# Optimization experiments

Measured on AMD Instinct MI355X. Metric: run time of the kernel, lower is better.

## Reference

```python
import jax, jax.numpy as jnp
import numpy as np

N = 50000      # nodes
E = 800000     # edges
D_IN = 128     # irreps_in dim
SH = 16        # irreps_sh dim (lmax=3)
EA = 16        # edge_attr_dim
H = 8          # num_heads
DQ = 64        # irreps_query dim (8 per head)
DK = 64        # irreps_key dim (8 per head)
DV = 128       # irreps_out dim (16 per head)
HID = 64       # radial MLP hidden


def setup_inputs() -> dict:
    key = jax.random.key(0)
    ks = jax.random.split(key, 20)
    g = lambda k, shape, fan: jax.random.normal(k, shape, jnp.float32) / np.sqrt(fan)
    return {
        "node_attr": jax.random.normal(ks[0], (N, D_IN), jnp.float32),
        "edge_attr": jax.random.normal(ks[1], (E, EA), jnp.float32),
        "edge_sh": jax.random.normal(ks[2], (E, SH), jnp.float32),
        # h_q linear
        "Wq": g(ks[3], (D_IN, DQ), D_IN),
        # h_k conv: depthwise SH mixing, channel-mixing linear, radial MLP gate
        "Wang_k": g(ks[4], (D_IN, SH), SH),
        "Wlin_k": g(ks[5], (D_IN, DK), D_IN),
        "W1k": g(ks[6], (EA, HID), EA),
        "b1k": jnp.zeros((HID,), jnp.float32),
        "W2k": g(ks[7], (HID, DK), HID),
        # h_v conv
        "Wang_v": g(ks[8], (D_IN, SH), SH),
        "Wlin_v": g(ks[9], (D_IN, DV), D_IN),
        "W1v": g(ks[10], (EA, HID), EA),
        "b1v": jnp.zeros((HID,), jnp.float32),
        "W2v": g(ks[11], (HID, DV), HID),
        # FullyConnectedTensorProduct(query_per_head, key_per_head, '0e') -> weighted bilinear dot
        "Wdot": g(ks[12], (DQ // H, DK // H), DQ // H),
        # lin_out
        "Wout": g(ks[13], (DV, DV), DV),
        "edge_index": jax.random.randint(ks[14], (2, E), 0, N, jnp.int64),
    }


def _conv_per_edge(x_src, edge_attr, edge_sh, Wang, Wlin, W1, b1, W2):
    # depthwise tensor product of node feats with edge SH, channel mix, radial gate
    rad = jax.nn.relu(edge_attr @ W1 + b1) @ W2          # [E, Dout]
    g = edge_sh @ Wang.T                                  # [E, D_IN]
    return ((x_src * g) @ Wlin) * rad                     # [E, Dout]


def reference(node_attr, edge_attr, edge_sh, Wq, Wang_k, Wlin_k, W1k, b1k, W2k,
              Wang_v, Wlin_v, W1v, b1v, W2v, Wdot, Wout, edge_index):
    src, dst = edge_index[0], edge_index[1]
    n = node_attr.shape[0]
    e = src.shape[0]

    q = (node_attr @ Wq).reshape(n, H, DQ // H)           # [N,H,dq]
    x_src = node_attr[src]                                # gather [E,D_IN]
    k = _conv_per_edge(x_src, edge_attr, edge_sh, Wang_k, Wlin_k, W1k, b1k, W2k).reshape(e, H, DK // H)
    v = _conv_per_edge(x_src, edge_attr, edge_sh, Wang_v, Wlin_v, W1v, b1v, W2v).reshape(e, H, DV // H)

    # TP 'dot' to scalars: weighted bilinear per head
    alpha = jnp.einsum('ehq,qk,ehk->eh', q[dst], Wdot, k)  # [E,H]

    # scatter_softmax over incoming edges of each dst node
    amax = jax.ops.segment_max(alpha, dst, num_segments=n)  # [N,H]
    ealpha = jnp.exp(alpha - amax[dst])
    denom = jax.ops.segment_sum(ealpha, dst, num_segments=n)
    attn = ealpha / denom[dst]                              # [E,H]

    # weighted scatter-sum of values
    out = jax.ops.segment_sum(attn[..., None] * v, dst, num_segments=n)  # [N,H,dv]
    return out.reshape(n, DV) @ Wout
```

## Files before the change

kernel.cpp:

```cpp
#include <hip/hip_runtime.h>
#include <stdint.h>

#define NN 50000
#define NE 800000
#define STRIP 49

typedef unsigned int u32;
typedef uint16_t u16;

__device__ __forceinline__ float b2f(u16 u){ return __builtin_bit_cast(float, (u32)((u32)u << 16)); }
__device__ __forceinline__ float b2f_lo(u32 p){ return __builtin_bit_cast(float, p << 16); }
__device__ __forceinline__ float b2f_hi(u32 p){ return __builtin_bit_cast(float, p & 0xffff0000u); }
__device__ __forceinline__ u32 f2b_bits(float f){ u32 u = __builtin_bit_cast(u32, f); return (u + 0x7fffu + ((u >> 16) & 1u)) >> 16; }
__device__ __forceinline__ u16 f2b(float f){ return (u16)f2b_bits(f); }
__device__ __forceinline__ u32 packb(float lo, float hi){
  u32 r;
  asm("v_cvt_pk_bf16_f32 %0, %1, %2" : "=v"(r) : "v"(lo), "v"(hi));
  return r;
}

typedef __bf16 bf16x2 __attribute__((ext_vector_type(2)));
#if defined(__has_builtin)
#if __has_builtin(__builtin_amdgcn_fdot2_f32_bf16)
#define HAVE_DOT2_BUILTIN 1
#endif
#endif

#ifdef HAVE_DOT2_BUILTIN
__device__ __forceinline__ float dot2b(u32 a, u32 b, float c){
  return __builtin_amdgcn_fdot2_f32_bf16(__builtin_bit_cast(bf16x2, a),
                                         __builtin_bit_cast(bf16x2, b), c, false);
}
#else
__device__ __forceinline__ float dot2b(u32 a, u32 b, float c){
  c = fmaf(b2f_lo(a), b2f_lo(b), c);
  return fmaf(b2f_hi(a), b2f_hi(b), c);
}
#endif

typedef __attribute__((ext_vector_type(8))) short short8;
typedef __attribute__((ext_vector_type(4))) float f32x4;
__device__ __forceinline__ f32x4 mf32(uint4 a, uint4 b, f32x4 c){
  return __builtin_amdgcn_mfma_f32_16x16x32_bf16(
      __builtin_bit_cast(short8, a), __builtin_bit_cast(short8, b), c, 0, 0, 0);
}

__device__ __forceinline__ int chperm(int n){
  return 32 * ((n & 63) >> 4) + 8 * ((n & 15) >> 2) + 4 * (n >> 6) + (n & 3);
}

#define OFF_WANG_V 0
#define OFF_W1_V   5120
#define OFF_WLIN_V 7680
#define OFF_W2_V   25088
#define OFF_WANG_K 34304
#define OFF_W1_K   39424
#define OFF_WLIN_K 41984
#define OFF_W2_K   50688
#define OFF_WOUT   55296
#define OFF_WQD    72704
#define WT_TOTAL   81408

__global__ __launch_bounds__(256) void zero_kernel(int* __restrict__ counts)
{
  int i = blockIdx.x * 256 + threadIdx.x;
  if (i < NN) counts[i] = 0;
}

__global__ __launch_bounds__(256) void prep_w_kernel(
    const float* __restrict__ Wang_v, const float* __restrict__ W1_v,
    const float* __restrict__ Wlin_v, const float* __restrict__ W2_v,
    const float* __restrict__ Wang_k, const float* __restrict__ W1_k,
    const float* __restrict__ Wlin_k, const float* __restrict__ W2_k,
    const float* __restrict__ Wout, const float* __restrict__ Wq,
    const float* __restrict__ Wdot,
    u16* __restrict__ wt)
{
  int idx = blockIdx.x * 256 + threadIdx.x;
  if (idx >= WT_TOTAL) return;
  float val = 0.f;
  if (idx < OFF_W1_V) {
    int l = idx - OFF_WANG_V, n = l / 40, k = l % 40;
    if (k >= 16 && k < 32) val = Wang_v[chperm(n) * 16 + (k - 16)];
  } else if (idx < OFF_WLIN_V) {
    int l = idx - OFF_W1_V, n = l / 40, k = l % 40;
    if (k < 16) val = W1_v[k * 64 + n];
  } else if (idx < OFF_W2_V) {
    int l = idx - OFF_WLIN_V, n = l / 136, k = l % 136;
    if (k < 128) val = Wlin_v[k * 128 + chperm(n)];
  } else if (idx < OFF_WANG_K) {
    int l = idx - OFF_W2_V, n = l / 72, k = l % 72;
    if (k < 64) val = W2_v[k * 128 + chperm(n)];
  } else if (idx < OFF_W1_K) {
    int l = idx - OFF_WANG_K, n = l / 40, k = l % 40;
    if (k >= 16 && k < 32) val = Wang_k[chperm(n) * 16 + (k - 16)];
  } else if (idx < OFF_WLIN_K) {
    int l = idx - OFF_W1_K, n = l / 40, k = l % 40;
    if (k < 16) val = W1_k[k * 64 + n];
  } else if (idx < OFF_W2_K) {
    int l = idx - OFF_WLIN_K, n = l / 136, k = l % 136;
    if (k < 128) val = Wlin_k[k * 64 + n];
  } else if (idx < OFF_WOUT) {
    int l = idx - OFF_W2_K, n = l / 72, k = l % 72;
    if (k < 64) val = W2_k[k * 64 + n];
  } else if (idx < OFF_WQD) {
    int l = idx - OFF_WOUT, n = l / 136, k = l % 136;
    if (k < 128) val = Wout[k * 128 + n];
  } else {
    int l = idx - OFF_WQD, n = l / 136, k = l % 136;
    if (k < 128) {
      int h = n >> 3, r = n & 7;
      float s = 0.f;
#pragma unroll
      for (int i = 0; i < 8; ++i) s += Wq[k * 64 + h * 8 + i] * Wdot[i * 8 + r];
      val = s;
    }
  }
  wt[idx] = f2b(val);
}

__global__ __launch_bounds__(256) void qw_kernel(const float* __restrict__ node_attr,
                                                 const u16* __restrict__ wt,
                                                 u16* __restrict__ qw)
{
  __shared__ __align__(16) u16 sX[64 * 136];
  uint4* sX4 = (uint4*)sX;
  u32* sX32 = (u32*)sX;
  const uint4* wt4 = (const uint4*)wt;
  const int tid = threadIdx.x, wv = tid >> 6, lane = tid & 63, lq = lane >> 4, ln = lane & 15;
  const int n0 = blockIdx.x * 64;
  uint4 rB[4];
#pragma unroll
  for (int ks = 0; ks < 4; ++ks) rB[ks] = wt4[9088 + (wv * 16 + ln) * 17 + ks * 4 + lq];
  {
    int row = tid >> 2, q4 = tid & 3;
    int n = n0 + row;
    bool valid = n < NN;
    const float4* xp = (const float4*)(node_attr + (size_t)(valid ? n : 0) * 128);
#pragma unroll
    for (int i = 0; i < 8; ++i) {
      float4 v = valid ? xp[q4 * 8 + i] : make_float4(0.f, 0.f, 0.f, 0.f);
      sX32[row * 68 + (q4 * 8 + i) * 2]     = packb(v.x, v.y);
      sX32[row * 68 + (q4 * 8 + i) * 2 + 1] = packb(v.z, v.w);
    }
  }
  __syncthreads();
  const f32x4 z4 = {0.f, 0.f, 0.f, 0.f};
  int col = wv * 16 + ln;
#pragma unroll
  for (int et = 0; et < 4; ++et) {
    f32x4 acc = z4;
#pragma unroll
    for (int ks = 0; ks < 4; ++ks) acc = mf32(sX4[(et * 16 + ln) * 17 + ks * 4 + lq], rB[ks], acc);
#pragma unroll
    for (int r = 0; r < 4; ++r) {
      int rr = n0 + et * 16 + lq * 4 + r;
      if (rr < NN) qw[(size_t)rr * 64 + col] = f2b(acc[r]);
    }
  }
}

__global__ __launch_bounds__(256) void count_kernel(const int* __restrict__ edge_index,
                                                    int* __restrict__ counts)
{
  int e = blockIdx.x * 256 + threadIdx.x;
  if (e < NE) { int d = edge_index[NE + e]; if ((u32)d >= NN) d = 0; atomicAdd(&counts[d], 1); }
}

__global__ __launch_bounds__(1024) void scan_kernel(const int* __restrict__ counts,
                                                    int* __restrict__ row_ptr,
                                                    int* __restrict__ cursor)
{
  __shared__ int s[1024];
  int tid = threadIdx.x;
  int base = tid * STRIP;
  int sum = 0;
  for (int i = 0; i < STRIP; ++i) { int idx = base + i; sum += (idx < NN) ? counts[idx] : 0; }
  s[tid] = sum;
  __syncthreads();
  for (int off = 1; off < 1024; off <<= 1) {
    int v = s[tid];
    int add = (tid >= off) ? s[tid - off] : 0;
    __syncthreads();
    s[tid] = v + add;
    __syncthreads();
  }
  int running = (tid == 0) ? 0 : s[tid - 1];
  for (int i = 0; i < STRIP; ++i) {
    int idx = base + i;
    if (idx < NN) { row_ptr[idx] = running; cursor[idx] = running; running += counts[idx]; }
  }
  if (tid == 1023) row_ptr[NN] = running;
}

__global__ __launch_bounds__(256) void fill_kernel(const int* __restrict__ edge_index,
                                                   int* __restrict__ cursor,
                                                   int* __restrict__ edge_pos)
{
  int e = blockIdx.x * 256 + threadIdx.x;
  if (e < NE) {
    int dst = edge_index[NE + e]; if ((u32)dst >= NN) dst = 0;
    int pos = atomicAdd(&cursor[dst], 1);
    edge_pos[e] = ((u32)pos < NE) ? pos : 0;
  }
}

__global__ __launch_bounds__(256, 2) void conv_fused_kernel(
    const float* __restrict__ node_attr, const float* __restrict__ edge_attr,
    const float* __restrict__ edge_sh, const int* __restrict__ edge_index,
    const float* __restrict__ b1v, const float* __restrict__ b1k,
    const u16* __restrict__ wt, const u16* __restrict__ qw,
    const int* __restrict__ edge_pos,
    u16* __restrict__ v_out, float* __restrict__ alpha)
{
  __shared__ __align__(16) u16 sC[64 * 40];
  __shared__ __align__(16) u16 sX[64 * 136];
  __shared__ __align__(16) u16 sTk[64 * 136];
  __shared__ __align__(16) u16 sHv[64 * 72];
  __shared__ __align__(16) u16 sHk[64 * 72];
  uint4* sC4 = (uint4*)sC; u32* sC32 = (u32*)sC;
  uint4* sX4 = (uint4*)sX;
  uint4* sTk4 = (uint4*)sTk;
  uint4* sHv4 = (uint4*)sHv;
  uint4* sHk4 = (uint4*)sHk;
  const uint4* wt4 = (const uint4*)wt;

  const int tid = threadIdx.x;
  const int wv = tid >> 6, lane = tid & 63, lq = lane >> 4, ln = lane & 15;
  const int e0 = blockIdx.x * 64;
  const int nA = wv * 16 + ln, nB = (wv + 4) * 16 + ln;
  const int cb  = wv * 16 + 4 * lq;
  const int cb8 = wv * 32 + 8 * lq;

  const int el = tid >> 2, p = tid & 3;
  int dq = edge_index[NE + e0 + el]; if ((u32)dq >= NN) dq = 0;
  const uint4* qptr = (const uint4*)(qw + (size_t)dq * 64 + p * 16);
  uint4 q0 = qptr[0], q1 = qptr[1];
  int pos_el = edge_pos[e0 + el]; if ((u32)pos_el >= NE) pos_el = 0;

  int srcs[4];
#pragma unroll
  for (int et = 0; et < 4; ++et) {
    int s = edge_index[e0 + et * 16 + ln];
    if ((u32)s >= NN) s = 0;
    srcs[et] = s;
  }

  uint4 rW1V    = wt4[640 + nA * 5 + lq];
  uint4 rW1K    = wt4[4928 + nA * 5 + lq];
  uint4 rWangV0 = wt4[nA * 5 + lq],        rWangV1 = wt4[nB * 5 + lq];
  uint4 rWangK0 = wt4[4288 + nA * 5 + lq], rWangK1 = wt4[4288 + nB * 5 + lq];
  float4 bV = *(const float4*)(b1v + cb);
  float4 bK = *(const float4*)(b1k + cb);

  {
    int r = tid >> 2, kq = tid & 3;
    float4 ea = ((const float4*)(edge_attr + (size_t)(e0 + r) * 16))[kq];
    *(uint2*)(sC32 + r * 20 + kq * 2) = make_uint2(packb(ea.x, ea.y), packb(ea.z, ea.w));
    float4 sh = ((const float4*)(edge_sh + (size_t)(e0 + r) * 16))[kq];
    *(uint2*)(sC32 + r * 20 + 8 + kq * 2) = make_uint2(packb(sh.x, sh.y), packb(sh.z, sh.w));
  }
  const float* xp0 = node_attr + (size_t)srcs[0] * 128 + cb8;
  float4 xa = *(const float4*)xp0;
  float4 xb = *(const float4*)(xp0 + 4);
  __syncthreads();

  const f32x4 z4 = {0.f, 0.f, 0.f, 0.f};
#pragma unroll
  for (int et = 0; et < 4; ++et) {
    float4 xa_n, xb_n;
    if (et < 3) {
      const float* xp = node_attr + (size_t)srcs[et + 1] * 128 + cb8;
      xa_n = *(const float4*)xp;
      xb_n = *(const float4*)(xp + 4);
    }
    uint4 aC = sC4[(et * 16 + ln) * 5 + lq];
    f32x4 hv  = mf32(rW1V, aC, z4);
    f32x4 hk  = mf32(rW1K, aC, z4);
    f32x4 t0v = mf32(rWangV0, aC, z4);
    f32x4 t1v = mf32(rWangV1, aC, z4);
    f32x4 t0k = mf32(rWangK0, aC, z4);
    f32x4 t1k = mf32(rWangK1, aC, z4);
    const int edge = et * 16 + ln;
    sX4[edge * 17 + 4 * wv + lq] = make_uint4(
        packb(t0v[0] * xa.x, t0v[1] * xa.y), packb(t0v[2] * xa.z, t0v[3] * xa.w),
        packb(t1v[0] * xb.x, t1v[1] * xb.y), packb(t1v[2] * xb.z, t1v[3] * xb.w));
    sTk4[edge * 17 + 4 * wv + lq] = make_uint4(
        packb(t0k[0] * xa.x, t0k[1] * xa.y), packb(t0k[2] * xa.z, t0k[3] * xa.w),
        packb(t1k[0] * xb.x, t1k[1] * xb.y), packb(t1k[2] * xb.z, t1k[3] * xb.w));
    *(uint2*)(sHv + edge * 72 + cb) = make_uint2(
        packb(fmaxf(hv[0] + bV.x, 0.f), fmaxf(hv[1] + bV.y, 0.f)),
        packb(fmaxf(hv[2] + bV.z, 0.f), fmaxf(hv[3] + bV.w, 0.f)));
    *(uint2*)(sHk + edge * 72 + cb) = make_uint2(
        packb(fmaxf(hk[0] + bK.x, 0.f), fmaxf(hk[1] + bK.y, 0.f)),
        packb(fmaxf(hk[2] + bK.z, 0.f), fmaxf(hk[3] + bK.w, 0.f)));
    xa = xa_n; xb = xb_n;
  }

  uint4 rWlinV[2][4], rWlinK[4], rW2V[2][2], rW2K[2];
#pragma unroll
  for (int ks = 0; ks < 4; ++ks) {
    rWlinV[0][ks] = wt4[960 + nA * 17 + ks * 4 + lq];
    rWlinV[1][ks] = wt4[960 + nB * 17 + ks * 4 + lq];
    rWlinK[ks]    = wt4[5248 + nA * 17 + ks * 4 + lq];
  }
#pragma unroll
  for (int ks = 0; ks < 2; ++ks) {
    rW2V[0][ks] = wt4[3136 + nA * 9 + ks * 4 + lq];
    rW2V[1][ks] = wt4[3136 + nB * 9 + ks * 4 + lq];
    rW2K[ks]    = wt4[6336 + nA * 9 + ks * 4 + lq];
  }
  __syncthreads();

  uint4 pv[4]; uint2 pk[4];
#pragma unroll
  for (int et = 0; et < 4; ++et) {
    const int er = et * 16 + ln;
    f32x4 acc0 = z4, acc1 = z4, acck = z4;
#pragma unroll
    for (int ks = 0; ks < 4; ++ks) {
      uint4 tb = sX4[er * 17 + ks * 4 + lq];
      acc0 = mf32(rWlinV[0][ks], tb, acc0);
      acc1 = mf32(rWlinV[1][ks], tb, acc1);
      acck = mf32(rWlinK[ks], sTk4[er * 17 + ks * 4 + lq], acck);
    }
    f32x4 b0 = z4, b1 = z4, bk = z4;
#pragma unroll
    for (int ks = 0; ks < 2; ++ks) {
      uint4 hb = sHv4[er * 9 + ks * 4 + lq];
      b0 = mf32(rW2V[0][ks], hb, b0);
      b1 = mf32(rW2V[1][ks], hb, b1);
      bk = mf32(rW2K[ks], sHk4[er * 9 + ks * 4 + lq], bk);
    }
    pv[et] = make_uint4(packb(acc0[0] * b0[0], acc0[1] * b0[1]),
                        packb(acc0[2] * b0[2], acc0[3] * b0[3]),
                        packb(acc1[0] * b1[0], acc1[1] * b1[1]),
                        packb(acc1[2] * b1[2], acc1[3] * b1[3]));
    pk[et] = make_uint2(packb(acck[0] * bk[0], acck[1] * bk[1]),
                        packb(acck[2] * bk[2], acck[3] * bk[3]));
  }
  __syncthreads();

#pragma unroll
  for (int et = 0; et < 4; ++et) {
    const int edge = et * 16 + ln;
    sX4[edge * 17 + 4 * wv + lq] = pv[et];
    *(uint2*)(sHk + edge * 72 + cb) = pk[et];
  }
  __syncthreads();

  {
    int row = tid >> 2, seg = tid & 3;
    uint4* gp = (uint4*)(v_out + (size_t)pos_el * 128);
#pragma unroll
    for (int i = 0; i < 4; ++i) gp[seg * 4 + i] = sX4[row * 17 + seg * 4 + i];
  }
  {
    uint4 k0 = sHk4[el * 9 + p * 2];
    uint4 k1 = sHk4[el * 9 + p * 2 + 1];
    float a0 = 0.f, a1 = 0.f;
    a0 = dot2b(q0.x, k0.x, a0); a0 = dot2b(q0.y, k0.y, a0);
    a0 = dot2b(q0.z, k0.z, a0); a0 = dot2b(q0.w, k0.w, a0);
    a1 = dot2b(q1.x, k1.x, a1); a1 = dot2b(q1.y, k1.y, a1);
    a1 = dot2b(q1.z, k1.z, a1); a1 = dot2b(q1.w, k1.w, a1);
    ((float2*)(alpha + (size_t)pos_el * 8))[p] = make_float2(a0, a1);
  }
}

#define OUPD(aa, ww)                                                   \
  { float mn = fmaxf(m, (aa));                                         \
    float sc = __expf(m - mn);                                         \
    float pw = __expf((aa) - mn);                                      \
    l = l * sc + pw;                                                   \
    accA = accA * sc + pw * b2f_lo(ww);                                \
    accB = accB * sc + pw * b2f_hi(ww);                                \
    m = mn; }

__global__ __launch_bounds__(256) void out_kernel(
    const int* __restrict__ row_ptr,
    const float* __restrict__ alpha, const u16* __restrict__ v_e,
    const u16* __restrict__ wt, float* __restrict__ out)
{
  __shared__ __align__(16) u16 sAgg[16 * 136];
  u32* sAgg32 = (u32*)sAgg;
  uint4* sAgg4 = (uint4*)sAgg;
  const uint4* wt4 = (const uint4*)wt;
  const u32* v32 = (const u32*)v_e;
  const int tid = threadIdx.x, wv = tid >> 6, lane = tid & 63, lq = lane >> 4, ln = lane & 15;
  const f32x4 z4 = {0.f, 0.f, 0.f, 0.f};
  uint4 rWT[2][4];
#pragma unroll
  for (int c = 0; c < 2; ++c) {
    int n = (wv * 2 + c) * 16 + ln;
#pragma unroll
    for (int ks = 0; ks < 4; ++ks) rWT[c][ks] = wt4[6912 + n * 17 + ks * 4 + lq];
  }
  const int hh = lane >> 3;
  const int grp = blockIdx.x;
#pragma unroll 1
  for (int i = 0; i < 4; ++i) {
    int n = grp * 16 + wv * 4 + i;
    int beg = row_ptr[n], end = row_ptr[n + 1];
    if (beg < 0) beg = 0; if (beg > NE) beg = NE;
    if (end < beg) end = beg; if (end > NE) end = NE;
    int deg = end - beg;
    float m = -3.0e38f, l = 0.f, accA = 0.f, accB = 0.f;
    int j = 0;
#pragma unroll 1
    for (; j + 4 <= deg; j += 4) {
      size_t b = (size_t)(beg + j);
      float a0 = alpha[(b)     * 8 + hh]; u32 w0 = v32[(b)     * 64 + lane];
      float a1 = alpha[(b + 1) * 8 + hh]; u32 w1 = v32[(b + 1) * 64 + lane];
      float a2 = alpha[(b + 2) * 8 + hh]; u32 w2 = v32[(b + 2) * 64 + lane];
      float a3 = alpha[(b + 3) * 8 + hh]; u32 w3 = v32[(b + 3) * 64 + lane];
      OUPD(a0, w0); OUPD(a1, w1); OUPD(a2, w2); OUPD(a3, w3);
    }
#pragma unroll 1
    for (; j < deg; ++j) {
      size_t b = (size_t)(beg + j);
      float a = alpha[b * 8 + hh]; u32 w = v32[b * 64 + lane];
      OUPD(a, w);
    }
    float inv = (l > 0.f) ? (1.f / l) : 0.f;
    accA *= inv; accB *= inv;
    sAgg32[(wv * 4 + i) * 68 + lane] = packb(accA, accB);
  }
  __syncthreads();
#pragma unroll
  for (int c = 0; c < 2; ++c) {
    f32x4 acc = z4;
#pragma unroll
    for (int ks = 0; ks < 4; ++ks) acc = mf32(sAgg4[ln * 17 + ks * 4 + lq], rWT[c][ks], acc);
    int col = (wv * 2 + c) * 16 + ln;
#pragma unroll
    for (int r = 0; r < 4; ++r)
      out[(size_t)(grp * 16 + lq * 4 + r) * 128 + col] = acc[r];
  }
}

extern "C" void kernel_launch(void* const* d_in, const int* in_sizes, int n_in,
                              void* d_out, int out_size, void* d_ws, size_t ws_size,
                              hipStream_t stream)
{
  const float* node_attr = (const float*)d_in[0];
  const float* edge_attr = (const float*)d_in[1];
  const float* edge_sh   = (const float*)d_in[2];
  const float* Wq        = (const float*)d_in[3];
  const float* Wang_k    = (const float*)d_in[4];
  const float* Wlin_k    = (const float*)d_in[5];
  const float* W1k       = (const float*)d_in[6];
  const float* b1k       = (const float*)d_in[7];
  const float* W2k       = (const float*)d_in[8];
  const float* Wang_v    = (const float*)d_in[9];
  const float* Wlin_v    = (const float*)d_in[10];
  const float* W1v       = (const float*)d_in[11];
  const float* b1v       = (const float*)d_in[12];
  const float* W2v       = (const float*)d_in[13];
  const float* Wdot      = (const float*)d_in[14];
  const float* Wout      = (const float*)d_in[15];
  const int* edge_index  = (const int*)d_in[16];
  float* out = (float*)d_out;

  char* ws = (char*)d_ws;
  u16*   v_e      = (u16*)(ws + 0);
  float* alpha    = (float*)(ws + 204800000);
  u16*   qw       = (u16*)(ws + 230400000);
  int*   counts   = (int*)(ws + 236800000);
  int*   row_ptr  = (int*)(ws + 237000064);
  int*   cursor   = (int*)(ws + 237200128);
  int*   edge_pos = (int*)(ws + 237400192);
  u16*   wt       = (u16*)(ws + 240600192);

  zero_kernel<<<dim3((NN + 255) / 256), dim3(256), 0, stream>>>(counts);
  prep_w_kernel<<<dim3((WT_TOTAL + 255) / 256), dim3(256), 0, stream>>>(
      Wang_v, W1v, Wlin_v, W2v, Wang_k, W1k, Wlin_k, W2k, Wout, Wq, Wdot, wt);
  qw_kernel<<<dim3((NN + 63) / 64), dim3(256), 0, stream>>>(node_attr, wt, qw);
  count_kernel<<<dim3((NE + 255) / 256), dim3(256), 0, stream>>>(edge_index, counts);
  scan_kernel<<<dim3(1), dim3(1024), 0, stream>>>(counts, row_ptr, cursor);
  fill_kernel<<<dim3((NE + 255) / 256), dim3(256), 0, stream>>>(edge_index, cursor, edge_pos);
  conv_fused_kernel<<<dim3(NE / 64), dim3(256), 0, stream>>>(
      node_attr, edge_attr, edge_sh, edge_index, b1v, b1k, wt, qw, edge_pos, v_e, alpha);
  out_kernel<<<dim3(3125), dim3(256), 0, stream>>>(row_ptr, alpha, v_e, wt, out);
}
```

Before: 642.6 us.

## Load edge attr/sh MFMA operands directly into registers, drop staging LDS buffer

Each lane now loads its edge_attr/edge_sh fragment for the MFMA A-operand straight from global memory into registers, packed to bf16. This removes the shared sC staging buffer and its __syncthreads. The launch bound is raised to 3 blocks per CU to use the freed LDS and get more occupancy. The cost is more register pressure and redundant global loads, since four wavefronts each load the same 64 edges, and the tighter register cap may cause spills.

```diff
diff --git a/kernel.cpp b/kernel.cpp
--- a/kernel.cpp
+++ b/kernel.cpp
@@ -205,7 +205,7 @@
   }
 }
 
-__global__ __launch_bounds__(256, 2) void conv_fused_kernel(
+__global__ __launch_bounds__(256, 3) void conv_fused_kernel(
     const float* __restrict__ node_attr, const float* __restrict__ edge_attr,
     const float* __restrict__ edge_sh, const int* __restrict__ edge_index,
     const float* __restrict__ b1v, const float* __restrict__ b1k,
@@ -213,12 +213,10 @@
     const int* __restrict__ edge_pos,
     u16* __restrict__ v_out, float* __restrict__ alpha)
 {
-  __shared__ __align__(16) u16 sC[64 * 40];
   __shared__ __align__(16) u16 sX[64 * 136];
   __shared__ __align__(16) u16 sTk[64 * 136];
   __shared__ __align__(16) u16 sHv[64 * 72];
   __shared__ __align__(16) u16 sHk[64 * 72];
-  uint4* sC4 = (uint4*)sC; u32* sC32 = (u32*)sC;
   uint4* sX4 = (uint4*)sX;
   uint4* sTk4 = (uint4*)sTk;
   uint4* sHv4 = (uint4*)sHv;
@@ -246,6 +244,17 @@
     srcs[et] = s;
   }
 
+  uint4 aC[4];
+#pragma unroll
+  for (int et = 0; et < 4; ++et) {
+    size_t eg = (size_t)(e0 + et * 16 + ln);
+    const float* cp = (lq < 2 ? edge_attr : edge_sh) + eg * 16 + (lq & 1) * 8;
+    float4 c0 = *(const float4*)cp;
+    float4 c1 = *(const float4*)(cp + 4);
+    aC[et] = make_uint4(packb(c0.x, c0.y), packb(c0.z, c0.w),
+                        packb(c1.x, c1.y), packb(c1.z, c1.w));
+  }
+
   uint4 rW1V    = wt4[640 + nA * 5 + lq];
   uint4 rW1K    = wt4[4928 + nA * 5 + lq];
   uint4 rWangV0 = wt4[nA * 5 + lq],        rWangV1 = wt4[nB * 5 + lq];
@@ -253,17 +262,9 @@
   float4 bV = *(const float4*)(b1v + cb);
   float4 bK = *(const float4*)(b1k + cb);
 
-  {
-    int r = tid >> 2, kq = tid & 3;
-    float4 ea = ((const float4*)(edge_attr + (size_t)(e0 + r) * 16))[kq];
-    *(uint2*)(sC32 + r * 20 + kq * 2) = make_uint2(packb(ea.x, ea.y), packb(ea.z, ea.w));
-    float4 sh = ((const float4*)(edge_sh + (size_t)(e0 + r) * 16))[kq];
-    *(uint2*)(sC32 + r * 20 + 8 + kq * 2) = make_uint2(packb(sh.x, sh.y), packb(sh.z, sh.w));
-  }
   const float* xp0 = node_attr + (size_t)srcs[0] * 128 + cb8;
   float4 xa = *(const float4*)xp0;
   float4 xb = *(const float4*)(xp0 + 4);
-  __syncthreads();
 
   const f32x4 z4 = {0.f, 0.f, 0.f, 0.f};
 #pragma unroll
@@ -274,13 +275,12 @@
       xa_n = *(const float4*)xp;
       xb_n = *(const float4*)(xp + 4);
     }
-    uint4 aC = sC4[(et * 16 + ln) * 5 + lq];
-    f32x4 hv  = mf32(rW1V, aC, z4);
-    f32x4 hk  = mf32(rW1K, aC, z4);
-    f32x4 t0v = mf32(rWangV0, aC, z4);
-    f32x4 t1v = mf32(rWangV1, aC, z4);
-    f32x4 t0k = mf32(rWangK0, aC, z4);
-    f32x4 t1k = mf32(rWangK1, aC, z4);
+    f32x4 hv  = mf32(rW1V, aC[et], z4);
+    f32x4 hk  = mf32(rW1K, aC[et], z4);
+    f32x4 t0v = mf32(rWangV0, aC[et], z4);
+    f32x4 t1v = mf32(rWangV1, aC[et], z4);
+    f32x4 t0k = mf32(rWangK0, aC[et], z4);
+    f32x4 t1k = mf32(rWangK1, aC[et], z4);
     const int edge = et * 16 + ln;
     sX4[edge * 17 + 4 * wv + lq] = make_uint4(
         packb(t0v[0] * xa.x, t0v[1] * xa.y), packb(t0v[2] * xa.z, t0v[3] * xa.w),
```

New measurement: 678.6 us. 1.06x slower.

## Split online softmax into separate max/exp pass and weighted-sum kernel

Applied to the files above, without the earlier changes.

Replaces the online-softmax update inside the output kernel with a dedicated attn_kernel. That kernel computes the per-node max, writes exp weights back into alpha and stores the denominators. The weighted-sum kernel then does plain FMAs, which removes two exps and several rescaling multiplies per edge per lane. In exchange it adds a kernel launch and extra reads and writes of alpha (25.6MB), done by a thread-per-(node,head) pass with strided, uncoalesced access. The denominators reuse the qw buffer region, which is dead by then.

```diff
diff --git a/kernel.cpp b/kernel.cpp
--- a/kernel.cpp
+++ b/kernel.cpp
@@ -367,18 +367,31 @@
   }
 }
 
-#define OUPD(aa, ww)                                                   \
-  { float mn = fmaxf(m, (aa));                                         \
-    float sc = __expf(m - mn);                                         \
-    float pw = __expf((aa) - mn);                                      \
-    l = l * sc + pw;                                                   \
-    accA = accA * sc + pw * b2f_lo(ww);                                \
-    accB = accB * sc + pw * b2f_hi(ww);                                \
-    m = mn; }
-
-__global__ __launch_bounds__(256) void out_kernel(
+__global__ __launch_bounds__(256) void attn_kernel(
+    const int* __restrict__ row_ptr, float* __restrict__ alpha,
+    float* __restrict__ denom)
+{
+  int t = blockIdx.x * 256 + threadIdx.x;
+  int n = t >> 3, h = t & 7;
+  if (n >= NN) return;
+  int beg = row_ptr[n], end = row_ptr[n + 1];
+  if (beg < 0) beg = 0; if (beg > NE) beg = NE;
+  if (end < beg) end = beg; if (end > NE) end = NE;
+  float m = -3.0e38f;
+  for (int j = beg; j < end; ++j) m = fmaxf(m, alpha[(size_t)j * 8 + h]);
+  float l = 0.f;
+  for (int j = beg; j < end; ++j) {
+    float w = __expf(alpha[(size_t)j * 8 + h] - m);
+    alpha[(size_t)j * 8 + h] = w;
+    l += w;
+  }
+  denom[(size_t)n * 8 + h] = l;
+}
+
+__global__ __launch_bounds__(256) void wsum_kernel(
     const int* __restrict__ row_ptr,
     const float* __restrict__ alpha, const u16* __restrict__ v_e,
+    const float* __restrict__ denom,
     const u16* __restrict__ wt, float* __restrict__ out)
 {
   __shared__ __align__(16) u16 sAgg[16 * 136];
@@ -404,23 +417,27 @@
     if (beg < 0) beg = 0; if (beg > NE) beg = NE;
     if (end < beg) end = beg; if (end > NE) end = NE;
     int deg = end - beg;
-    float m = -3.0e38f, l = 0.f, accA = 0.f, accB = 0.f;
+    float accA = 0.f, accB = 0.f;
     int j = 0;
 #pragma unroll 1
     for (; j + 4 <= deg; j += 4) {
       size_t b = (size_t)(beg + j);
-      float a0 = alpha[(b)     * 8 + hh]; u32 w0 = v32[(b)     * 64 + lane];
-      float a1 = alpha[(b + 1) * 8 + hh]; u32 w1 = v32[(b + 1) * 64 + lane];
-      float a2 = alpha[(b + 2) * 8 + hh]; u32 w2 = v32[(b + 2) * 64 + lane];
-      float a3 = alpha[(b + 3) * 8 + hh]; u32 w3 = v32[(b + 3) * 64 + lane];
-      OUPD(a0, w0); OUPD(a1, w1); OUPD(a2, w2); OUPD(a3, w3);
+      float w0 = alpha[(b)     * 8 + hh]; u32 x0 = v32[(b)     * 64 + lane];
+      float w1 = alpha[(b + 1) * 8 + hh]; u32 x1 = v32[(b + 1) * 64 + lane];
+      float w2 = alpha[(b + 2) * 8 + hh]; u32 x2 = v32[(b + 2) * 64 + lane];
+      float w3 = alpha[(b + 3) * 8 + hh]; u32 x3 = v32[(b + 3) * 64 + lane];
+      accA = fmaf(w0, b2f_lo(x0), accA); accB = fmaf(w0, b2f_hi(x0), accB);
+      accA = fmaf(w1, b2f_lo(x1), accA); accB = fmaf(w1, b2f_hi(x1), accB);
+      accA = fmaf(w2, b2f_lo(x2), accA); accB = fmaf(w2, b2f_hi(x2), accB);
+      accA = fmaf(w3, b2f_lo(x3), accA); accB = fmaf(w3, b2f_hi(x3), accB);
     }
 #pragma unroll 1
     for (; j < deg; ++j) {
       size_t b = (size_t)(beg + j);
-      float a = alpha[b * 8 + hh]; u32 w = v32[b * 64 + lane];
-      OUPD(a, w);
-    }
+      float w = alpha[b * 8 + hh]; u32 x = v32[b * 64 + lane];
+      accA = fmaf(w, b2f_lo(x), accA); accB = fmaf(w, b2f_hi(x), accB);
+    }
+    float l = denom[(size_t)n * 8 + hh];
     float inv = (l > 0.f) ? (1.f / l) : 0.f;
     accA *= inv; accB *= inv;
     sAgg32[(wv * 4 + i) * 68 + lane] = packb(accA, accB);
@@ -465,6 +482,7 @@
   u16*   v_e      = (u16*)(ws + 0);
   float* alpha    = (float*)(ws + 204800000);
   u16*   qw       = (u16*)(ws + 230400000);
+  float* denom    = (float*)(ws + 230400000);
   int*   counts   = (int*)(ws + 236800000);
   int*   row_ptr  = (int*)(ws + 237000064);
   int*   cursor   = (int*)(ws + 237200128);
@@ -480,5 +498,6 @@
   fill_kernel<<<dim3((NE + 255) / 256), dim3(256), 0, stream>>>(edge_index, cursor, edge_pos);
   conv_fused_kernel<<<dim3(NE / 64), dim3(256), 0, stream>>>(
       node_attr, edge_attr, edge_sh, edge_index, b1v, b1k, wt, qw, edge_pos, v_e, alpha);
-  out_kernel<<<dim3(3125), dim3(256), 0, stream>>>(row_ptr, alpha, v_e, wt, out);
-}
+  attn_kernel<<<dim3((NN * 8 + 255) / 256), dim3(256), 0, stream>>>(row_ptr, alpha, denom);
+  wsum_kernel<<<dim3(3125), dim3(256), 0, stream>>>(row_ptr, alpha, v_e, denom, wt, out);
+}
```

Result: slower. 661.2 us (+2.9%).

## Fuse CSR slot assignment into conv kernel and split online-softmax chains

Applied to the files above, without the earlier changes.

Removes the separate fill kernel and the edge_pos array: each conv block now claims its CSR slots with atomicAdd on the cursor and shares them through LDS before scattering v and alpha. This drops one kernel launch plus the edge_pos write and read. Separately, out_kernel keeps two independent online-softmax accumulators, interleaved across edges and merged at the end, to shorten the serial exp/FMA dependency chain. The atomics now sit inside the heavier conv kernel and may add latency there.

```diff
diff --git a/kernel.cpp b/kernel.cpp
--- a/kernel.cpp
+++ b/kernel.cpp
@@ -193,24 +193,12 @@
   if (tid == 1023) row_ptr[NN] = running;
 }
 
-__global__ __launch_bounds__(256) void fill_kernel(const int* __restrict__ edge_index,
-                                                   int* __restrict__ cursor,
-                                                   int* __restrict__ edge_pos)
-{
-  int e = blockIdx.x * 256 + threadIdx.x;
-  if (e < NE) {
-    int dst = edge_index[NE + e]; if ((u32)dst >= NN) dst = 0;
-    int pos = atomicAdd(&cursor[dst], 1);
-    edge_pos[e] = ((u32)pos < NE) ? pos : 0;
-  }
-}
-
 __global__ __launch_bounds__(256, 2) void conv_fused_kernel(
     const float* __restrict__ node_attr, const float* __restrict__ edge_attr,
     const float* __restrict__ edge_sh, const int* __restrict__ edge_index,
     const float* __restrict__ b1v, const float* __restrict__ b1k,
     const u16* __restrict__ wt, const u16* __restrict__ qw,
-    const int* __restrict__ edge_pos,
+    int* __restrict__ cursor,
     u16* __restrict__ v_out, float* __restrict__ alpha)
 {
   __shared__ __align__(16) u16 sC[64 * 40];
@@ -218,6 +206,7 @@
   __shared__ __align__(16) u16 sTk[64 * 136];
   __shared__ __align__(16) u16 sHv[64 * 72];
   __shared__ __align__(16) u16 sHk[64 * 72];
+  __shared__ int sPos[64];
   uint4* sC4 = (uint4*)sC; u32* sC32 = (u32*)sC;
   uint4* sX4 = (uint4*)sX;
   uint4* sTk4 = (uint4*)sTk;
@@ -234,9 +223,9 @@
 
   const int el = tid >> 2, p = tid & 3;
   int dq = edge_index[NE + e0 + el]; if ((u32)dq >= NN) dq = 0;
+  if (p == 0) sPos[el] = atomicAdd(&cursor[dq], 1);
   const uint4* qptr = (const uint4*)(qw + (size_t)dq * 64 + p * 16);
   uint4 q0 = qptr[0], q1 = qptr[1];
-  int pos_el = edge_pos[e0 + el]; if ((u32)pos_el >= NE) pos_el = 0;
 
   int srcs[4];
 #pragma unroll
@@ -351,11 +340,13 @@
 
   {
     int row = tid >> 2, seg = tid & 3;
-    uint4* gp = (uint4*)(v_out + (size_t)pos_el * 128);
+    int pos = sPos[row]; if ((u32)pos >= NE) pos = 0;
+    uint4* gp = (uint4*)(v_out + (size_t)pos * 128);
 #pragma unroll
     for (int i = 0; i < 4; ++i) gp[seg * 4 + i] = sX4[row * 17 + seg * 4 + i];
   }
   {
+    int pos_el = sPos[el]; if ((u32)pos_el >= NE) pos_el = 0;
     uint4 k0 = sHk4[el * 9 + p * 2];
     uint4 k1 = sHk4[el * 9 + p * 2 + 1];
     float a0 = 0.f, a1 = 0.f;
@@ -367,14 +358,14 @@
   }
 }
 
-#define OUPD(aa, ww)                                                   \
-  { float mn = fmaxf(m, (aa));                                         \
-    float sc = __expf(m - mn);                                         \
+#define OUPD(mm_, ll_, aA_, aB_, aa, ww)                               \
+  { float mn = fmaxf(mm_, (aa));                                       \
+    float sc = __expf(mm_ - mn);                                       \
     float pw = __expf((aa) - mn);                                      \
-    l = l * sc + pw;                                                   \
-    accA = accA * sc + pw * b2f_lo(ww);                                \
-    accB = accB * sc + pw * b2f_hi(ww);                                \
-    m = mn; }
+    ll_ = ll_ * sc + pw;                                               \
+    aA_ = aA_ * sc + pw * b2f_lo(ww);                                  \
+    aB_ = aB_ * sc + pw * b2f_hi(ww);                                  \
+    mm_ = mn; }
 
 __global__ __launch_bounds__(256) void out_kernel(
     const int* __restrict__ row_ptr,
@@ -404,23 +395,32 @@
     if (beg < 0) beg = 0; if (beg > NE) beg = NE;
     if (end < beg) end = beg; if (end > NE) end = NE;
     int deg = end - beg;
-    float m = -3.0e38f, l = 0.f, accA = 0.f, accB = 0.f;
+    float m0 = -3.0e38f, l0 = 0.f, a0A = 0.f, a0B = 0.f;
+    float m1 = -3.0e38f, l1 = 0.f, a1A = 0.f, a1B = 0.f;
     int j = 0;
 #pragma unroll 1
     for (; j + 4 <= deg; j += 4) {
       size_t b = (size_t)(beg + j);
-      float a0 = alpha[(b)     * 8 + hh]; u32 w0 = v32[(b)     * 64 + lane];
-      float a1 = alpha[(b + 1) * 8 + hh]; u32 w1 = v32[(b + 1) * 64 + lane];
-      float a2 = alpha[(b + 2) * 8 + hh]; u32 w2 = v32[(b + 2) * 64 + lane];
-      float a3 = alpha[(b + 3) * 8 + hh]; u32 w3 = v32[(b + 3) * 64 + lane];
-      OUPD(a0, w0); OUPD(a1, w1); OUPD(a2, w2); OUPD(a3, w3);
+      float aa0 = alpha[(b)     * 8 + hh]; u32 w0 = v32[(b)     * 64 + lane];
+      float aa1 = alpha[(b + 1) * 8 + hh]; u32 w1 = v32[(b + 1) * 64 + lane];
+      float aa2 = alpha[(b + 2) * 8 + hh]; u32 w2 = v32[(b + 2) * 64 + lane];
+      float aa3 = alpha[(b + 3) * 8 + hh]; u32 w3 = v32[(b + 3) * 64 + lane];
+      OUPD(m0, l0, a0A, a0B, aa0, w0);
+      OUPD(m1, l1, a1A, a1B, aa1, w1);
+      OUPD(m0, l0, a0A, a0B, aa2, w2);
+      OUPD(m1, l1, a1A, a1B, aa3, w3);
     }
 #pragma unroll 1
     for (; j < deg; ++j) {
       size_t b = (size_t)(beg + j);
-      float a = alpha[b * 8 + hh]; u32 w = v32[b * 64 + lane];
-      OUPD(a, w);
-    }
+      float aa = alpha[b * 8 + hh]; u32 w = v32[b * 64 + lane];
+      OUPD(m0, l0, a0A, a0B, aa, w);
+    }
+    float mm = fmaxf(m0, m1);
+    float s0 = __expf(m0 - mm), s1 = __expf(m1 - mm);
+    float l = l0 * s0 + l1 * s1;
+    float accA = a0A * s0 + a1A * s1;
+    float accB = a0B * s0 + a1B * s1;
     float inv = (l > 0.f) ? (1.f / l) : 0.f;
     accA *= inv; accB *= inv;
     sAgg32[(wv * 4 + i) * 68 + lane] = packb(accA, accB);
@@ -468,7 +468,6 @@
   int*   counts   = (int*)(ws + 236800000);
   int*   row_ptr  = (int*)(ws + 237000064);
   int*   cursor   = (int*)(ws + 237200128);
-  int*   edge_pos = (int*)(ws + 237400192);
   u16*   wt       = (u16*)(ws + 240600192);
 
   zero_kernel<<<dim3((NN + 255) / 256), dim3(256), 0, stream>>>(counts);
@@ -477,8 +476,7 @@
   qw_kernel<<<dim3((NN + 63) / 64), dim3(256), 0, stream>>>(node_attr, wt, qw);
   count_kernel<<<dim3((NE + 255) / 256), dim3(256), 0, stream>>>(edge_index, counts);
   scan_kernel<<<dim3(1), dim3(1024), 0, stream>>>(counts, row_ptr, cursor);
-  fill_kernel<<<dim3((NE + 255) / 256), dim3(256), 0, stream>>>(edge_index, cursor, edge_pos);
   conv_fused_kernel<<<dim3(NE / 64), dim3(256), 0, stream>>>(
-      node_attr, edge_attr, edge_sh, edge_index, b1v, b1k, wt, qw, edge_pos, v_e, alpha);
+      node_attr, edge_attr, edge_sh, edge_index, b1v, b1k, wt, qw, cursor, v_e, alpha);
   out_kernel<<<dim3(3125), dim3(256), 0, stream>>>(row_ptr, alpha, v_e, wt, out);
 }
```

New measurement: 637.2 us. Within noise of the previous version (-0.8%).
